# Kernel tuning notes

Hardware: AMD Instinct MI355X
Metric: run time of the kernel (lower is better)

## Reference

```python
import jax, jax.numpy as jnp
import numpy as np

B, L, D = 4, 1024, 1024
H, DK, DV = 16, 64, 64
HID = 4 * D
EPS = 1e-5


def layer_norm(x, w, b):
    m = x.mean(-1, keepdims=True)
    v = ((x - m) ** 2).mean(-1, keepdims=True)
    return (x - m) * jax.lax.rsqrt(v + EPS) * w + b


def sln(hl, w, ln_w, ln_b, gamma, beta):
    # Self-modulated LayerNorm: gamma * w * LN(hl) + beta * w
    return gamma * w * layer_norm(hl, ln_w, ln_b) + beta * w


def setup_inputs() -> dict:
    key = jax.random.key(0)
    ks = jax.random.split(key, 20)
    s = 0.02
    inp = {
        "q": jax.random.normal(ks[0], (B, L, D), jnp.float32),
        "k": jax.random.normal(ks[1], (B, L, D), jnp.float32),
        "v": jax.random.normal(ks[2], (B, L, D), jnp.float32),
        "z": jax.random.normal(ks[3], (B, L, D), jnp.float32),
        # projections stored [in, out] (torch Linear applies x @ W.T + b)
        "wq_w": jax.random.normal(ks[4], (D, H * DK), jnp.float32) * s,
        "wq_b": jnp.zeros((H * DK,), jnp.float32),
        "wk_w": jax.random.normal(ks[5], (D, H * DK), jnp.float32) * s,
        "wk_b": jnp.zeros((H * DK,), jnp.float32),
        "wv_w": jax.random.normal(ks[6], (D, H * DV), jnp.float32) * s,
        "wv_b": jnp.zeros((H * DV,), jnp.float32),
        "fc_w": jax.random.normal(ks[7], (H * DV, D), jnp.float32) * s,
        "fc_b": jnp.zeros((D,), jnp.float32),
        "mlp1_w": jax.random.normal(ks[8], (D, HID), jnp.float32) * s,
        "mlp1_b": jnp.zeros((HID,), jnp.float32),
        "mlp2_w": jax.random.normal(ks[9], (HID, D), jnp.float32) * s,
        "mlp2_b": jnp.zeros((D,), jnp.float32),
        "ln1_w": jnp.ones((D,), jnp.float32),
        "ln1_b": jnp.zeros((D,), jnp.float32),
        "g1": jax.random.normal(ks[10], (1, 1, 1), jnp.float32),
        "b1": jax.random.normal(ks[11], (1, 1, 1), jnp.float32),
        "ln2_w": jnp.ones((D,), jnp.float32),
        "ln2_b": jnp.zeros((D,), jnp.float32),
        "g2": jax.random.normal(ks[12], (1, 1, 1), jnp.float32),
        "b2": jax.random.normal(ks[13], (1, 1, 1), jnp.float32),
    }
    return inp


def reference(q, k, v, z,
              wq_w, wq_b, wk_w, wk_b, wv_w, wv_b, fc_w, fc_b,
              mlp1_w, mlp1_b, mlp2_w, mlp2_b,
              ln1_w, ln1_b, g1, b1, ln2_w, ln2_b, g2, b2):
    scale = 1.0 / np.sqrt(DK).astype(np.float32)
    q = sln(q, z, ln1_w, ln1_b, g1, b1)
    residual = q
    qh = (q @ wq_w + wq_b).reshape(B, L, H, DK)
    kh = (k @ wk_w + wk_b).reshape(B, L, H, DK)
    vh = (v @ wv_w + wv_b).reshape(B, L, H, DV)
    # scores per (head, batch) matching torch layout (n_head*sz_b, Lq, Lk)
    attn = jnp.einsum("bqhd,bkhd->hbqk", qh, kh) * scale
    attn = jax.nn.softmax(attn, axis=-1)
    out = jnp.einsum("hbqk,bkhd->bqhd", attn, vh).reshape(B, L, H * DV)
    out = out @ fc_w + fc_b
    out = out + residual
    h = sln(out, z, ln2_w, ln2_b, g2, b2)
    h = jax.nn.gelu(h @ mlp1_w + mlp1_b, approximate=False)
    out = (h @ mlp2_w + mlp2_b) + out
    return out, attn.reshape(H * B, L, L)
```

## Files before the change

kernel.cpp:

```cpp
#include <hip/hip_runtime.h>
#include <math.h>

namespace {

constexpr int kL  = 1024;
constexpr int kD  = 1024;
constexpr int kB  = 4;
constexpr int kH  = 16;
constexpr int kDK = 64;
constexpr int kHID = 4096;

typedef unsigned short ushort_t;
typedef short  s16x8 __attribute__((ext_vector_type(8)));
typedef float  f32x4 __attribute__((ext_vector_type(4)));
typedef unsigned short u16x4 __attribute__((ext_vector_type(4)));

__device__ __forceinline__ ushort_t f2bf(float f) {
    unsigned u = __float_as_uint(f);
    unsigned r = u + 0x7fffu + ((u >> 16) & 1u);
    return (ushort_t)(r >> 16);
}

__device__ __forceinline__ void gld16(const void* g, void* l) {
    __builtin_amdgcn_global_load_lds((__attribute__((address_space(1))) void*)(g),
                                     (__attribute__((address_space(3))) void*)(l),
                                     16, 0, 0);
}

__device__ __forceinline__ float wred_sum(float v) {
    #pragma unroll
    for (int o = 32; o > 0; o >>= 1) v += __shfl_xor(v, o, 64);
    return v;
}

__global__ __launch_bounds__(256) void sln_kernel(
    const float* __restrict__ x, const float* __restrict__ x2, float* __restrict__ xw,
    const float* __restrict__ z,
    const float* __restrict__ lnw, const float* __restrict__ lnb,
    const float* __restrict__ g, const float* __restrict__ bt,
    float* __restrict__ outf, ushort_t* __restrict__ outb)
{
    const int row = blockIdx.x;
    const int tid = threadIdx.x;
    const size_t base = (size_t)row * kD;
    float4 xv = ((const float4*)(x + base))[tid];
    if (x2) {
        float4 a = ((const float4*)(x2 + base))[tid];
        xv.x += a.x; xv.y += a.y; xv.z += a.z; xv.w += a.w;
    }
    if (xw) ((float4*)(xw + base))[tid] = xv;
    float s  = xv.x + xv.y + xv.z + xv.w;
    float sq = xv.x * xv.x + xv.y * xv.y + xv.z * xv.z + xv.w * xv.w;
    __shared__ float r1[4], r2[4];
    float ws = wred_sum(s), wq = wred_sum(sq);
    int lane = tid & 63, wid = tid >> 6;
    if (lane == 0) { r1[wid] = ws; r2[wid] = wq; }
    __syncthreads();
    float st = r1[0] + r1[1] + r1[2] + r1[3];
    float qt = r2[0] + r2[1] + r2[2] + r2[3];
    float mean = st * (1.0f / kD);
    float var  = qt * (1.0f / kD) - mean * mean;
    float rs = rsqrtf(var + 1e-5f);
    float gv = g[0], bv = bt[0];
    float4 zv = ((const float4*)(z + base))[tid];
    float4 wv = ((const float4*)lnw)[tid];
    float4 lb = ((const float4*)lnb)[tid];
    float4 o;
    o.x = zv.x * (gv * ((xv.x - mean) * rs * wv.x + lb.x) + bv);
    o.y = zv.y * (gv * ((xv.y - mean) * rs * wv.y + lb.y) + bv);
    o.z = zv.z * (gv * ((xv.z - mean) * rs * wv.z + lb.z) + bv);
    o.w = zv.w * (gv * ((xv.w - mean) * rs * wv.w + lb.w) + bv);
    if (outf) ((float4*)(outf + base))[tid] = o;
    u16x4 ob; ob[0] = f2bf(o.x); ob[1] = f2bf(o.y); ob[2] = f2bf(o.z); ob[3] = f2bf(o.w);
    ((u16x4*)(outb + base))[tid] = ob;
}

__global__ __launch_bounds__(256) void cvt2_bf16(
    const float* __restrict__ kx, const float* __restrict__ vx, ushort_t* __restrict__ kv)
{
    int b = blockIdx.x;
    bool isv = b >= 4096;
    const float* src = isv ? vx : kx;
    ushort_t* dst = kv + (isv ? (size_t)4194304 : 0);
    int i = (b & 4095) * 256 + threadIdx.x;
    f32x4 v = ((const f32x4*)src)[i];
    u16x4 o; o[0] = f2bf(v[0]); o[1] = f2bf(v[1]); o[2] = f2bf(v[2]); o[3] = f2bf(v[3]);
    ((u16x4*)dst)[i] = o;
}

__global__ __launch_bounds__(256) void addf4(
    float* __restrict__ dst, const float* __restrict__ src)
{
    int i = blockIdx.x * 256 + threadIdx.x;
    f32x4 d = ((const f32x4*)dst)[i];
    f32x4 s = ((const f32x4*)src)[i];
    d[0] += s[0]; d[1] += s[1]; d[2] += s[2]; d[3] += s[3];
    ((f32x4*)dst)[i] = d;
}

__global__ __launch_bounds__(256) void twcvt(
    const float* __restrict__ src, ushort_t* __restrict__ dst, int R, int C)
{
    __shared__ float t[32][33];
    int c0 = blockIdx.x * 32, r0 = blockIdx.y * 32;
    int tx = threadIdx.x & 31, ty = threadIdx.x >> 5;
    #pragma unroll
    for (int i = 0; i < 4; i++) {
        int r = ty + i * 8;
        t[r][tx] = src[(size_t)(r0 + r) * C + c0 + tx];
    }
    __syncthreads();
    #pragma unroll
    for (int i = 0; i < 4; i++) {
        int c = ty + i * 8;
        dst[(size_t)(c0 + c) * R + r0 + tx] = f2bf(t[tx][c]);
    }
}

__global__ __launch_bounds__(256) void twcvt4(
    const float* __restrict__ s0, const float* __restrict__ s1,
    const float* __restrict__ s2, const float* __restrict__ s3,
    ushort_t* __restrict__ dst)
{
    __shared__ float t[32][33];
    int zz = blockIdx.z;
    const float* src = zz == 0 ? s0 : zz == 1 ? s1 : zz == 2 ? s2 : s3;
    ushort_t* d = dst + (size_t)zz * 1048576;
    int c0 = blockIdx.x * 32, r0 = blockIdx.y * 32;
    int tx = threadIdx.x & 31, ty = threadIdx.x >> 5;
    #pragma unroll
    for (int i = 0; i < 4; i++) {
        int r = ty + i * 8;
        t[r][tx] = src[(size_t)(r0 + r) * 1024 + c0 + tx];
    }
    __syncthreads();
    #pragma unroll
    for (int i = 0; i < 4; i++) {
        int c = ty + i * 8;
        d[(size_t)(c0 + c) * 1024 + r0 + tx] = f2bf(t[tx][c]);
    }
}

__global__ __launch_bounds__(256) void vtrans(
    const ushort_t* __restrict__ vh, ushort_t* __restrict__ vhT)
{
    __shared__ ushort_t t[32][33];
    int p = blockIdx.z, b = p & 3, h = p >> 2;
    int j0 = blockIdx.x * 32, d0 = blockIdx.y * 32;
    int tx = threadIdx.x & 31, ty = threadIdx.x >> 5;
    const ushort_t* src = vh + (size_t)b * (kL * kD) + h * kDK;
    #pragma unroll
    for (int i = 0; i < 4; i++) {
        int j = ty + i * 8;
        t[j][tx] = src[(size_t)(j0 + j) * kD + d0 + tx];
    }
    __syncthreads();
    ushort_t* dst = vhT + (size_t)p * (kDK * kL);
    #pragma unroll
    for (int i = 0; i < 4; i++) {
        int d = ty + i * 8;
        dst[(size_t)(d0 + d) * kL + j0 + tx] = t[tx][d];
    }
}

__global__ __launch_bounds__(256) void mgemm(
    const ushort_t* __restrict__ A, int lda,
    const ushort_t* __restrict__ Bt, int ldb,
    void* __restrict__ Cv, int ldc, int K,
    const float* __restrict__ bias, const float* __restrict__ res,
    float scale, int flags, int mode,
    const float* __restrict__ bias1, const float* __restrict__ bias2,
    void* __restrict__ Cv2)
{
    __shared__ __align__(16) ushort_t As[128 * 32];
    __shared__ __align__(16) ushort_t Bs[128 * 32];
    if (mode == 2) {
        int z = blockIdx.z;
        A  += (size_t)z * (4096u * 1024u);
        Bt += (size_t)z * (1024u * 1024u);
        Cv = (void*)((ushort_t*)Cv + (size_t)z * (4096u * 1024u));
        if (z == 1) bias = bias1;
        else if (z == 2) bias = bias2;
    } else if (mode == 3) {
        int z = blockIdx.z;
        A  += (size_t)z * K;
        Bt += (size_t)z * K;
        if (z == 1) { Cv = Cv2; bias = nullptr; res = nullptr; flags = 0; }
    }
    float*    Cf = (float*)Cv;
    ushort_t* Cb = (ushort_t*)Cv;
    const int nx = gridDim.x, nwg = nx * gridDim.y;
    int f = blockIdx.y * nx + blockIdx.x;
    int rr = (f & 7) * (nwg >> 3) + (f >> 3);
    const int bx = rr % nx, by = rr / nx;
    const int tid = threadIdx.x;
    const int lane = tid & 63, w = tid >> 6;
    const int m0 = by * 128, n0 = bx * 128;
    const int r0 = tid >> 2;
    const int c0 = (tid & 3) ^ (r0 & 3);
    const ushort_t* Ag0 = A  + (size_t)(m0 + r0) * lda + c0 * 8;
    const ushort_t* Ag1 = Ag0 + (size_t)64 * lda;
    const ushort_t* Bg0 = Bt + (size_t)(n0 + r0) * ldb + c0 * 8;
    const ushort_t* Bg1 = Bg0 + (size_t)64 * ldb;
    char* AsW = (char*)As + w * 1024;
    char* BsW = (char*)Bs + w * 1024;
    const int wm = (w & 1) * 64, wn = (w >> 1) * 64;
    const int fn = lane & 15, q = lane >> 4;
    int aoff[4], boff[4];
    #pragma unroll
    for (int i = 0; i < 4; i++) {
        int ra = wm + i * 16 + fn;
        aoff[i] = (ra * 4 + (q ^ (ra & 3))) * 16;
        int rb = wn + i * 16 + fn;
        boff[i] = (rb * 4 + (q ^ (rb & 3))) * 16;
    }
    f32x4 acc[4][4] = {};
    for (int k0 = 0; k0 < K; k0 += 32) {
        gld16(Ag0 + k0, AsW);
        gld16(Ag1 + k0, AsW + 4096);
        gld16(Bg0 + k0, BsW);
        gld16(Bg1 + k0, BsW + 4096);
        __syncthreads();
        s16x8 af[4], bfr[4];
        #pragma unroll
        for (int i = 0; i < 4; i++) {
            af[i]  = *(const s16x8*)((const char*)As + aoff[i]);
            bfr[i] = *(const s16x8*)((const char*)Bs + boff[i]);
        }
        #pragma unroll
        for (int mi = 0; mi < 4; mi++)
            #pragma unroll
            for (int ni = 0; ni < 4; ni++)
                acc[mi][ni] = __builtin_amdgcn_mfma_f32_16x16x32_bf16(
                    af[mi], bfr[ni], acc[mi][ni], 0, 0, 0);
        __syncthreads();
    }
    #pragma unroll
    for (int mi = 0; mi < 4; mi++) {
        #pragma unroll
        for (int ni = 0; ni < 4; ni++) {
            #pragma unroll
            for (int r = 0; r < 4; r++) {
                int gm = m0 + wm + mi * 16 + q * 4 + r;
                int gn = n0 + wn + ni * 16 + fn;
                float v = acc[mi][ni][r] * scale;
                if (bias) v += bias[gn];
                if (flags & 1) v = 0.5f * v * (1.0f + erff(v * 0.70710678118654752f));
                if (res) v += res[(size_t)gm * ldc + gn];
                if (flags & 2) Cb[(size_t)gm * ldc + gn] = f2bf(v);
                else           Cf[(size_t)gm * ldc + gn] = v;
            }
        }
    }
}

__global__ __launch_bounds__(512) void fused_attn(
    const ushort_t* __restrict__ qh, const ushort_t* __restrict__ kh,
    const ushort_t* __restrict__ vhT, float* __restrict__ attn,
    ushort_t* __restrict__ ctx)
{
    __shared__ __align__(16) char PlBuf[8 * 4096];
    __shared__ float redm[8][32];
    __shared__ float reds[8][32];
    const int orig = blockIdx.y * 32 + blockIdx.x;
    const int nf = (orig & 7) * 256 + (orig >> 3);
    const int p = nf >> 5, b = p & 3, h = p >> 2;
    const int m0 = (nf & 31) * 32;
    const int tid = threadIdx.x;
    const int lane = tid & 63, w = tid >> 6;
    const int fn = lane & 15, q = lane >> 4;
    const ushort_t* Qb = qh + (size_t)b * (kL * kD) + h * 64;
    const ushort_t* Kb = kh + (size_t)b * (kL * kD) + h * 64;
    float* Pp = attn + (size_t)p * kL * kL;

    f32x4 acc[2][8] = {};
    #pragma unroll
    for (int kk = 0; kk < 2; kk++) {
        s16x8 aq[2], bq[8];
        #pragma unroll
        for (int mi = 0; mi < 2; mi++)
            aq[mi] = *(const s16x8*)(Qb + (size_t)(m0 + mi * 16 + fn) * kD + kk * 32 + q * 8);
        #pragma unroll
        for (int ni = 0; ni < 8; ni++)
            bq[ni] = *(const s16x8*)(Kb + (size_t)(w * 128 + ni * 16 + fn) * kD + kk * 32 + q * 8);
        #pragma unroll
        for (int mi = 0; mi < 2; mi++)
            #pragma unroll
            for (int ni = 0; ni < 8; ni++)
                acc[mi][ni] = __builtin_amdgcn_mfma_f32_16x16x32_bf16(
                    aq[mi], bq[ni], acc[mi][ni], 0, 0, 0);
    }

    float mloc[2][4];
    #pragma unroll
    for (int mi = 0; mi < 2; mi++) {
        #pragma unroll
        for (int r = 0; r < 4; r++) {
            float m = -3.0e38f;
            #pragma unroll
            for (int ni = 0; ni < 8; ni++) {
                acc[mi][ni][r] *= 0.125f;
                m = fmaxf(m, acc[mi][ni][r]);
            }
            mloc[mi][r] = m;
        }
    }
    #pragma unroll
    for (int o = 1; o < 16; o <<= 1) {
        #pragma unroll
        for (int mi = 0; mi < 2; mi++)
            #pragma unroll
            for (int r = 0; r < 4; r++)
                mloc[mi][r] = fmaxf(mloc[mi][r], __shfl_xor(mloc[mi][r], o, 64));
    }
    if (fn == 0) {
        #pragma unroll
        for (int mi = 0; mi < 2; mi++)
            #pragma unroll
            for (int r = 0; r < 4; r++)
                redm[w][mi * 16 + q * 4 + r] = mloc[mi][r];
    }
    __syncthreads();
    #pragma unroll
    for (int mi = 0; mi < 2; mi++) {
        #pragma unroll
        for (int r = 0; r < 4; r++) {
            int row = mi * 16 + q * 4 + r;
            float m = redm[0][row];
            #pragma unroll
            for (int w2 = 1; w2 < 8; w2++) m = fmaxf(m, redm[w2][row]);
            float s = 0.f;
            #pragma unroll
            for (int ni = 0; ni < 8; ni++) {
                float e = __expf(acc[mi][ni][r] - m);
                acc[mi][ni][r] = e;
                s += e;
            }
            mloc[mi][r] = s;
        }
    }
    #pragma unroll
    for (int o = 1; o < 16; o <<= 1) {
        #pragma unroll
        for (int mi = 0; mi < 2; mi++)
            #pragma unroll
            for (int r = 0; r < 4; r++)
                mloc[mi][r] += __shfl_xor(mloc[mi][r], o, 64);
    }
    if (fn == 0) {
        #pragma unroll
        for (int mi = 0; mi < 2; mi++)
            #pragma unroll
            for (int r = 0; r < 4; r++)
                reds[w][mi * 16 + q * 4 + r] = mloc[mi][r];
    }
    __syncthreads();
    float inv[2][4];
    #pragma unroll
    for (int mi = 0; mi < 2; mi++) {
        #pragma unroll
        for (int r = 0; r < 4; r++) {
            int row = mi * 16 + q * 4 + r;
            float s = reds[0][row];
            #pragma unroll
            for (int w2 = 1; w2 < 8; w2++) s += reds[w2][row];
            inv[mi][r] = 1.0f / s;
        }
    }
    #pragma unroll
    for (int mi = 0; mi < 2; mi++)
        #pragma unroll
        for (int ni = 0; ni < 8; ni++)
            #pragma unroll
            for (int r = 0; r < 4; r++)
                __builtin_nontemporal_store(
                    acc[mi][ni][r] * inv[mi][r],
                    &Pp[(size_t)(m0 + mi * 16 + q * 4 + r) * kL + w * 128 + ni * 16 + fn]);

    const ushort_t* Vb = vhT + (size_t)p * (kDK * kL);
    char* Plw = PlBuf + w * 4096;
    f32x4 acc2[2][4] = {};
    #pragma unroll
    for (int half = 0; half < 2; half++) {
        #pragma unroll
        for (int mi = 0; mi < 2; mi++)
            #pragma unroll
            for (int ni = 0; ni < 4; ni++)
                #pragma unroll
                for (int r = 0; r < 4; r++) {
                    int row = mi * 16 + q * 4 + r;
                    int cl  = ni * 16 + fn;
                    *(ushort_t*)(Plw + ((row * 128 + cl * 2) ^ ((row & 7) << 4)))
                        = f2bf(acc[mi][half * 4 + ni][r]);
                }
        #pragma unroll
        for (int kh2 = 0; kh2 < 2; kh2++) {
            int kk = half * 2 + kh2;
            s16x8 pa[2];
            #pragma unroll
            for (int mi = 0; mi < 2; mi++) {
                int row = mi * 16 + fn;
                pa[mi] = *(const s16x8*)(Plw +
                    ((row * 128 + (kh2 * 32 + q * 8) * 2) ^ ((row & 7) << 4)));
            }
            #pragma unroll
            for (int nj = 0; nj < 4; nj++) {
                s16x8 bv = *(const s16x8*)(Vb + (size_t)(nj * 16 + fn) * kL +
                                           w * 128 + kk * 32 + q * 8);
                #pragma unroll
                for (int mi = 0; mi < 2; mi++)
                    acc2[mi][nj] = __builtin_amdgcn_mfma_f32_16x16x32_bf16(
                        pa[mi], bv, acc2[mi][nj], 0, 0, 0);
            }
        }
    }
    #pragma unroll
    for (int mi = 0; mi < 2; mi++)
        #pragma unroll
        for (int nj = 0; nj < 4; nj++)
            #pragma unroll
            for (int r = 0; r < 4; r++)
                acc2[mi][nj][r] *= inv[mi][r];

    __syncthreads();
    float (*cred)[2048] = (float (*)[2048])PlBuf;
    if (w < 4) {
        #pragma unroll
        for (int mi = 0; mi < 2; mi++)
            #pragma unroll
            for (int nj = 0; nj < 4; nj++)
                #pragma unroll
                for (int r = 0; r < 4; r++)
                    cred[w][(mi * 16 + q * 4 + r) * 64 + nj * 16 + fn] = acc2[mi][nj][r];
    }
    __syncthreads();
    if (w >= 4) {
        #pragma unroll
        for (int mi = 0; mi < 2; mi++)
            #pragma unroll
            for (int nj = 0; nj < 4; nj++)
                #pragma unroll
                for (int r = 0; r < 4; r++)
                    cred[w - 4][(mi * 16 + q * 4 + r) * 64 + nj * 16 + fn] += acc2[mi][nj][r];
    }
    __syncthreads();
    {
        int idx0 = tid * 4;
        int row = idx0 >> 6, d0 = idx0 & 63;
        f32x4 s0 = *(const f32x4*)&cred[0][idx0];
        #pragma unroll
        for (int wb = 1; wb < 4; wb++) {
            f32x4 t = *(const f32x4*)&cred[wb][idx0];
            s0[0] += t[0]; s0[1] += t[1]; s0[2] += t[2]; s0[3] += t[3];
        }
        u16x4 o;
        o[0] = f2bf(s0[0]); o[1] = f2bf(s0[1]); o[2] = f2bf(s0[2]); o[3] = f2bf(s0[3]);
        *(u16x4*)(ctx + (size_t)b * (kL * kD) + (size_t)(m0 + row) * kD + h * 64 + d0) = o;
    }
}

}

extern "C" void kernel_launch(void* const* d_in, const int* in_sizes, int n_in,
                              void* d_out, int out_size, void* d_ws, size_t ws_size,
                              hipStream_t stream)
{
    (void)in_sizes; (void)n_in; (void)out_size; (void)ws_size;
    const float* q      = (const float*)d_in[0];
    const float* k      = (const float*)d_in[1];
    const float* v      = (const float*)d_in[2];
    const float* z      = (const float*)d_in[3];
    const float* wq_w   = (const float*)d_in[4];
    const float* wq_b   = (const float*)d_in[5];
    const float* wk_w   = (const float*)d_in[6];
    const float* wk_b   = (const float*)d_in[7];
    const float* wv_w   = (const float*)d_in[8];
    const float* wv_b   = (const float*)d_in[9];
    const float* fc_w   = (const float*)d_in[10];
    const float* fc_b   = (const float*)d_in[11];
    const float* mlp1_w = (const float*)d_in[12];
    const float* mlp1_b = (const float*)d_in[13];
    const float* mlp2_w = (const float*)d_in[14];
    const float* mlp2_b = (const float*)d_in[15];
    const float* ln1_w  = (const float*)d_in[16];
    const float* ln1_b  = (const float*)d_in[17];
    const float* g1     = (const float*)d_in[18];
    const float* b1     = (const float*)d_in[19];
    const float* ln2_w  = (const float*)d_in[20];
    const float* ln2_b  = (const float*)d_in[21];
    const float* g2     = (const float*)d_in[22];
    const float* b2     = (const float*)d_in[23];

    float* out0 = (float*)d_out;
    float* attn = (float*)d_out + (size_t)kB * kL * kD;

    char* arena = (char*)d_ws;
    const size_t MB = 1u << 20;
    float*    qp   = (float*)(arena);
    ushort_t* qb   = (ushort_t*)(arena + 16 * MB);
    ushort_t* kb   = (ushort_t*)(arena + 24 * MB);
    ushort_t* vb   = (ushort_t*)(arena + 32 * MB);
    ushort_t* qh   = (ushort_t*)(arena + 40 * MB);
    ushort_t* kh   = (ushort_t*)(arena + 48 * MB);
    ushort_t* vh   = (ushort_t*)(arena + 56 * MB);
    ushort_t* vhT  = (ushort_t*)(arena + 32 * MB);
    ushort_t* ctx  = (ushort_t*)(arena + 56 * MB);
    float*    fcP  = (float*)(arena + 16 * MB);
    ushort_t* h2   = (ushort_t*)(arena + 32 * MB);
    float*    out1 = (float*)(arena + 64 * MB);
    ushort_t* hid  = (ushort_t*)(arena);
    float*    m2P  = (float*)(arena + 40 * MB);
    ushort_t* wqT  = (ushort_t*)(arena + 80 * MB);
    ushort_t* fcT  = (ushort_t*)(arena + 86 * MB);
    ushort_t* m1T  = (ushort_t*)(arena + 88 * MB);
    ushort_t* m2T  = (ushort_t*)(arena + 96 * MB);

    dim3 blk(256);
    twcvt4<<<dim3(32, 32, 4), blk, 0, stream>>>(wq_w, wk_w, wv_w, fc_w, wqT);
    twcvt<<<dim3(128, 32), blk, 0, stream>>>(mlp1_w, m1T, kD, kHID);
    twcvt<<<dim3(32, 128), blk, 0, stream>>>(mlp2_w, m2T, kHID, kD);
    cvt2_bf16<<<dim3(8192), blk, 0, stream>>>(k, v, kb);
    sln_kernel<<<dim3(kB * kL), blk, 0, stream>>>(q, nullptr, nullptr, z,
                                                  ln1_w, ln1_b, g1, b1, qp, qb);
    mgemm<<<dim3(8, 32, 3), blk, 0, stream>>>(qb, kD, wqT, kD, qh, kD, kD,
                                              wq_b, nullptr, 1.0f, 2, 2, wk_b, wv_b, nullptr);
    vtrans<<<dim3(32, 2, 64), blk, 0, stream>>>(vh, vhT);
    fused_attn<<<dim3(kL / 32, 64), dim3(512), 0, stream>>>(qh, kh, vhT, attn, ctx);
    mgemm<<<dim3(8, 32, 2), blk, 0, stream>>>(ctx, kD, fcT, kD, out1, kD, kD / 2,
                                              fc_b, qp, 1.0f, 0, 3, nullptr, nullptr, fcP);
    sln_kernel<<<dim3(kB * kL), blk, 0, stream>>>(out1, fcP, out1, z,
                                                  ln2_w, ln2_b, g2, b2, nullptr, h2);
    mgemm<<<dim3(32, 32, 1), blk, 0, stream>>>(h2, kD, m1T, kD, hid, kHID, kD,
                                               mlp1_b, nullptr, 1.0f, 3, 0, nullptr, nullptr, nullptr);
    mgemm<<<dim3(8, 32, 2), blk, 0, stream>>>(hid, kHID, m2T, kHID, out0, kD, kHID / 2,
                                              mlp2_b, out1, 1.0f, 0, 3, nullptr, nullptr, m2P);
    addf4<<<dim3(4096), blk, 0, stream>>>(out0, m2P);
}
```

Baseline: 780.6 us.

## Add 256x256 triple-buffered GEMM kernel and merge preprocessing launches

```diff
diff --git a/kernel.cpp b/kernel.cpp
--- a/kernel.cpp
+++ b/kernel.cpp
@@ -31,6 +31,94 @@
     #pragma unroll
     for (int o = 32; o > 0; o >>= 1) v += __shfl_xor(v, o, 64);
     return v;
+}
+
+__global__ __launch_bounds__(256) void prep(
+    const float* __restrict__ wq_w, const float* __restrict__ wk_w,
+    const float* __restrict__ wv_w, const float* __restrict__ fc_w,
+    ushort_t* __restrict__ wT4,
+    const float* __restrict__ mlp1_w, ushort_t* __restrict__ m1T,
+    const float* __restrict__ mlp2_w, ushort_t* __restrict__ m2T,
+    const float* __restrict__ kx, const float* __restrict__ vx, ushort_t* __restrict__ kv,
+    const float* __restrict__ q, const float* __restrict__ z,
+    const float* __restrict__ ln1w, const float* __restrict__ ln1b,
+    const float* __restrict__ g1, const float* __restrict__ b1,
+    float* __restrict__ qp, ushort_t* __restrict__ qb)
+{
+    __shared__ float t[32][33];
+    __shared__ float r1[4], r2[4];
+    const int b = blockIdx.x;
+    const int tid = threadIdx.x;
+    if (b < 12288) {
+        const float* src; ushort_t* dst; int R, C, bx, by;
+        if (b < 4096) {
+            int zz = b >> 10, idx = b & 1023;
+            src = zz == 0 ? wq_w : zz == 1 ? wk_w : zz == 2 ? wv_w : fc_w;
+            dst = wT4 + (size_t)zz * 1048576;
+            R = 1024; C = 1024; bx = idx & 31; by = idx >> 5;
+        } else if (b < 8192) {
+            int idx = b - 4096;
+            src = mlp1_w; dst = m1T; R = 1024; C = 4096;
+            bx = idx & 127; by = idx >> 7;
+        } else {
+            int idx = b - 8192;
+            src = mlp2_w; dst = m2T; R = 4096; C = 1024;
+            bx = idx & 31; by = idx >> 5;
+        }
+        int c0 = bx * 32, rr0 = by * 32;
+        int tx = tid & 31, ty = tid >> 5;
+        #pragma unroll
+        for (int i = 0; i < 4; i++) {
+            int r = ty + i * 8;
+            t[r][tx] = src[(size_t)(rr0 + r) * C + c0 + tx];
+        }
+        __syncthreads();
+        #pragma unroll
+        for (int i = 0; i < 4; i++) {
+            int c = ty + i * 8;
+            dst[(size_t)(c0 + c) * R + rr0 + tx] = f2bf(t[tx][c]);
+        }
+        return;
+    }
+    if (b < 20480) {
+        int bb = b - 12288;
+        bool isv = bb >= 4096;
+        const float* src = isv ? vx : kx;
+        ushort_t* dst = kv + (isv ? (size_t)4194304 : 0);
+        int i = (bb & 4095) * 256 + tid;
+        f32x4 v = ((const f32x4*)src)[i];
+        u16x4 o; o[0] = f2bf(v[0]); o[1] = f2bf(v[1]); o[2] = f2bf(v[2]); o[3] = f2bf(v[3]);
+        ((u16x4*)dst)[i] = o;
+        return;
+    }
+    {
+        const int row = b - 20480;
+        const size_t base = (size_t)row * kD;
+        float4 xv = ((const float4*)(q + base))[tid];
+        float s  = xv.x + xv.y + xv.z + xv.w;
+        float sq = xv.x * xv.x + xv.y * xv.y + xv.z * xv.z + xv.w * xv.w;
+        float ws = wred_sum(s), wq = wred_sum(sq);
+        int lane = tid & 63, wid = tid >> 6;
+        if (lane == 0) { r1[wid] = ws; r2[wid] = wq; }
+        __syncthreads();
+        float st = r1[0] + r1[1] + r1[2] + r1[3];
+        float qt = r2[0] + r2[1] + r2[2] + r2[3];
+        float mean = st * (1.0f / kD);
+        float var  = qt * (1.0f / kD) - mean * mean;
+        float rs = rsqrtf(var + 1e-5f);
+        float gv = g1[0], bv = b1[0];
+        float4 zv = ((const float4*)(z + base))[tid];
+        float4 wv = ((const float4*)ln1w)[tid];
+        float4 lb = ((const float4*)ln1b)[tid];
+        float4 o;
+        o.x = zv.x * (gv * ((xv.x - mean) * rs * wv.x + lb.x) + bv);
+        o.y = zv.y * (gv * ((xv.y - mean) * rs * wv.y + lb.y) + bv);
+        o.z = zv.z * (gv * ((xv.z - mean) * rs * wv.z + lb.z) + bv);
+        o.w = zv.w * (gv * ((xv.w - mean) * rs * wv.w + lb.w) + bv);
+        ((float4*)(qp + base))[tid] = o;
+        u16x4 ob; ob[0] = f2bf(o.x); ob[1] = f2bf(o.y); ob[2] = f2bf(o.z); ob[3] = f2bf(o.w);
+        ((u16x4*)(qb + base))[tid] = ob;
+    }
 }
 
 __global__ __launch_bounds__(256) void sln_kernel(
@@ -75,70 +163,18 @@
     ((u16x4*)(outb + base))[tid] = ob;
 }
 
-__global__ __launch_bounds__(256) void cvt2_bf16(
-    const float* __restrict__ kx, const float* __restrict__ vx, ushort_t* __restrict__ kv)
-{
-    int b = blockIdx.x;
-    bool isv = b >= 4096;
-    const float* src = isv ? vx : kx;
-    ushort_t* dst = kv + (isv ? (size_t)4194304 : 0);
-    int i = (b & 4095) * 256 + threadIdx.x;
-    f32x4 v = ((const f32x4*)src)[i];
-    u16x4 o; o[0] = f2bf(v[0]); o[1] = f2bf(v[1]); o[2] = f2bf(v[2]); o[3] = f2bf(v[3]);
-    ((u16x4*)dst)[i] = o;
-}
-
-__global__ __launch_bounds__(256) void addf4(
-    float* __restrict__ dst, const float* __restrict__ src)
+__global__ __launch_bounds__(256) void combine4(
+    float* __restrict__ dst, const float* __restrict__ p1,
+    const float* __restrict__ p2, const float* __restrict__ p3)
 {
     int i = blockIdx.x * 256 + threadIdx.x;
     f32x4 d = ((const f32x4*)dst)[i];
-    f32x4 s = ((const f32x4*)src)[i];
-    d[0] += s[0]; d[1] += s[1]; d[2] += s[2]; d[3] += s[3];
+    f32x4 a = ((const f32x4*)p1)[i];
+    f32x4 b = ((const f32x4*)p2)[i];
+    f32x4 c = ((const f32x4*)p3)[i];
+    d[0] += a[0] + b[0] + c[0]; d[1] += a[1] + b[1] + c[1];
+    d[2] += a[2] + b[2] + c[2]; d[3] += a[3] + b[3] + c[3];
     ((f32x4*)dst)[i] = d;
-}
-
-__global__ __launch_bounds__(256) void twcvt(
-    const float* __restrict__ src, ushort_t* __restrict__ dst, int R, int C)
-{
-    __shared__ float t[32][33];
-    int c0 = blockIdx.x * 32, r0 = blockIdx.y * 32;
-    int tx = threadIdx.x & 31, ty = threadIdx.x >> 5;
-    #pragma unroll
-    for (int i = 0; i < 4; i++) {
-        int r = ty + i * 8;
-        t[r][tx] = src[(size_t)(r0 + r) * C + c0 + tx];
-    }
-    __syncthreads();
-    #pragma unroll
-    for (int i = 0; i < 4; i++) {
-        int c = ty + i * 8;
-        dst[(size_t)(c0 + c) * R + r0 + tx] = f2bf(t[tx][c]);
-    }
-}
-
-__global__ __launch_bounds__(256) void twcvt4(
-    const float* __restrict__ s0, const float* __restrict__ s1,
-    const float* __restrict__ s2, const float* __restrict__ s3,
-    ushort_t* __restrict__ dst)
-{
-    __shared__ float t[32][33];
-    int zz = blockIdx.z;
-    const float* src = zz == 0 ? s0 : zz == 1 ? s1 : zz == 2 ? s2 : s3;
-    ushort_t* d = dst + (size_t)zz * 1048576;
-    int c0 = blockIdx.x * 32, r0 = blockIdx.y * 32;
-    int tx = threadIdx.x & 31, ty = threadIdx.x >> 5;
-    #pragma unroll
-    for (int i = 0; i < 4; i++) {
-        int r = ty + i * 8;
-        t[r][tx] = src[(size_t)(r0 + r) * 1024 + c0 + tx];
-    }
-    __syncthreads();
-    #pragma unroll
-    for (int i = 0; i < 4; i++) {
-        int c = ty + i * 8;
-        d[(size_t)(c0 + c) * 1024 + r0 + tx] = f2bf(t[tx][c]);
-    }
 }
 
 __global__ __launch_bounds__(256) void vtrans(
@@ -174,14 +210,7 @@
 {
     __shared__ __align__(16) ushort_t As[128 * 32];
     __shared__ __align__(16) ushort_t Bs[128 * 32];
-    if (mode == 2) {
-        int z = blockIdx.z;
-        A  += (size_t)z * (4096u * 1024u);
-        Bt += (size_t)z * (1024u * 1024u);
-        Cv = (void*)((ushort_t*)Cv + (size_t)z * (4096u * 1024u));
-        if (z == 1) bias = bias1;
-        else if (z == 2) bias = bias2;
-    } else if (mode == 3) {
+    if (mode == 3) {
         int z = blockIdx.z;
         A  += (size_t)z * K;
         Bt += (size_t)z * K;
@@ -243,6 +272,130 @@
             for (int r = 0; r < 4; r++) {
                 int gm = m0 + wm + mi * 16 + q * 4 + r;
                 int gn = n0 + wn + ni * 16 + fn;
+                float v = acc[mi][ni][r] * scale;
+                if (bias) v += bias[gn];
+                if (flags & 1) v = 0.5f * v * (1.0f + erff(v * 0.70710678118654752f));
+                if (res) v += res[(size_t)gm * ldc + gn];
+                if (flags & 2) Cb[(size_t)gm * ldc + gn] = f2bf(v);
+                else           Cf[(size_t)gm * ldc + gn] = v;
+            }
+        }
+    }
+}
+
+__global__ __launch_bounds__(512, 2) void g3(
+    const ushort_t* __restrict__ A, int lda,
+    const ushort_t* __restrict__ Bt, int ldb,
+    void* __restrict__ Cv, int ldc, int K,
+    const float* __restrict__ bias, const float* __restrict__ res,
+    float scale, int flags, int mode,
+    const float* __restrict__ bias1, const float* __restrict__ bias2,
+    float* __restrict__ Cv2, float* __restrict__ Cv3)
+{
+    __shared__ __align__(16) ushort_t As[3 * 8192];
+    __shared__ __align__(16) ushort_t Bs[3 * 8192];
+    if (mode == 2) {
+        int zz = blockIdx.z;
+        A  += (size_t)zz * (4096u * 1024u);
+        Bt += (size_t)zz * (1024u * 1024u);
+        Cv = (void*)((ushort_t*)Cv + (size_t)zz * (4096u * 1024u));
+        if (zz == 1) bias = bias1;
+        else if (zz == 2) bias = bias2;
+    } else if (mode == 4) {
+        int zz = blockIdx.z;
+        A  += (size_t)zz * K;
+        Bt += (size_t)zz * K;
+        if (zz > 0) {
+            Cv = (void*)(zz == 3 ? Cv3 : (Cv2 + (size_t)(zz - 1) * (4096u * 1024u)));
+            bias = nullptr; res = nullptr; flags = 0;
+        }
+    }
+    float*    Cf = (float*)Cv;
+    ushort_t* Cb = (ushort_t*)Cv;
+    const int nx = gridDim.x, nwg = nx * gridDim.y;
+    int f = blockIdx.y * nx + blockIdx.x;
+    int rr = (f & 7) * (nwg >> 3) + (f >> 3);
+    const int bx = rr % nx, by = rr / nx;
+    const int tid = threadIdx.x;
+    const int lane = tid & 63, w = tid >> 6;
+    const int wr = w >> 2, wc = w & 3;
+    const int fn = lane & 15, q = lane >> 4;
+    const int m0 = by * 256, n0 = bx * 256;
+    const int r0 = tid >> 2;
+    const int c0 = (tid & 3) ^ (r0 & 3);
+    const ushort_t* Ag = A  + (size_t)(m0 + r0) * lda + c0 * 8;
+    const ushort_t* Bg = Bt + (size_t)(n0 + r0) * ldb + c0 * 8;
+    char* AsB = (char*)As;
+    char* BsB = (char*)Bs;
+    const int sdst = w * 1024;
+    int aoff[8], boff[4];
+    #pragma unroll
+    for (int i = 0; i < 8; i++) {
+        int ra = wr * 128 + i * 16 + fn;
+        aoff[i] = ra * 64 + ((q ^ (ra & 3)) << 4);
+    }
+    #pragma unroll
+    for (int i = 0; i < 4; i++) {
+        int rb = wc * 64 + i * 16 + fn;
+        boff[i] = rb * 64 + ((q ^ (rb & 3)) << 4);
+    }
+    const int NT = K >> 5;
+    f32x4 acc[8][4] = {};
+
+    #define G3_STAGE(T, s_, h_)                                                   \
+        do {                                                                      \
+            gld16(Ag + (size_t)((h_) * 128) * lda + (size_t)(T) * 32,             \
+                  AsB + (s_) * 16384 + (h_) * 8192 + sdst);                       \
+            gld16(Bg + (size_t)((h_) * 128) * ldb + (size_t)(T) * 32,             \
+                  BsB + (s_) * 16384 + (h_) * 8192 + sdst);                       \
+        } while (0)
+
+    G3_STAGE(0, 0, 0); G3_STAGE(0, 0, 1);
+    G3_STAGE(1, 1, 0); G3_STAGE(1, 1, 1);
+    asm volatile("s_waitcnt vmcnt(4)" ::: "memory");
+    __builtin_amdgcn_s_barrier();
+    __builtin_amdgcn_sched_barrier(0);
+
+    int sT = 0, s2 = 2;
+    for (int T = 0; T < NT; ++T) {
+        if (T + 2 < NT) { G3_STAGE(T + 2, s2, 0); G3_STAGE(T + 2, s2, 1); }
+        const char* Asl = (const char*)As + sT * 16384;
+        const char* Bsl = (const char*)Bs + sT * 16384;
+        s16x8 af[8], bf[4];
+        #pragma unroll
+        for (int i = 0; i < 8; i++) af[i] = *(const s16x8*)(Asl + aoff[i]);
+        #pragma unroll
+        for (int i = 0; i < 4; i++) bf[i] = *(const s16x8*)(Bsl + boff[i]);
+        asm volatile("s_waitcnt lgkmcnt(0)" ::: "memory");
+        __builtin_amdgcn_sched_barrier(0);
+        __builtin_amdgcn_s_setprio(1);
+        #pragma unroll
+        for (int mi = 0; mi < 8; mi++)
+            #pragma unroll
+            for (int ni = 0; ni < 4; ni++)
+                acc[mi][ni] = __builtin_amdgcn_mfma_f32_16x16x32_bf16(
+                    af[mi], bf[ni], acc[mi][ni], 0, 0, 0);
+        __builtin_amdgcn_s_setprio(0);
+        __builtin_amdgcn_sched_barrier(0);
+        if (T + 1 < NT) {
+            if (T + 2 < NT) asm volatile("s_waitcnt vmcnt(4)" ::: "memory");
+            else            asm volatile("s_waitcnt vmcnt(0)" ::: "memory");
+            __builtin_amdgcn_s_barrier();
+            __builtin_amdgcn_sched_barrier(0);
+        }
+        sT = (sT == 2) ? 0 : sT + 1;
+        s2 = (s2 == 2) ? 0 : s2 + 1;
+    }
+    #undef G3_STAGE
+
+    #pragma unroll
+    for (int mi = 0; mi < 8; mi++) {
+        #pragma unroll
+        for (int ni = 0; ni < 4; ni++) {
+            #pragma unroll
+            for (int r = 0; r < 4; r++) {
+                int gm = m0 + wr * 128 + mi * 16 + q * 4 + r;
+                int gn = n0 + wc * 64 + ni * 16 + fn;
                 float v = acc[mi][ni][r] * scale;
                 if (bias) v += bias[gn];
                 if (flags & 1) v = 0.5f * v * (1.0f + erff(v * 0.70710678118654752f));
@@ -509,30 +662,32 @@
     ushort_t* h2   = (ushort_t*)(arena + 32 * MB);
     float*    out1 = (float*)(arena + 64 * MB);
     ushort_t* hid  = (ushort_t*)(arena);
-    float*    m2P  = (float*)(arena + 40 * MB);
-    ushort_t* wqT  = (ushort_t*)(arena + 80 * MB);
+    float*    p1   = (float*)(arena + 32 * MB);
+    float*    p3   = (float*)(arena + 80 * MB);
+    ushort_t* wT4  = (ushort_t*)(arena + 80 * MB);
     ushort_t* fcT  = (ushort_t*)(arena + 86 * MB);
     ushort_t* m1T  = (ushort_t*)(arena + 88 * MB);
     ushort_t* m2T  = (ushort_t*)(arena + 96 * MB);
 
     dim3 blk(256);
-    twcvt4<<<dim3(32, 32, 4), blk, 0, stream>>>(wq_w, wk_w, wv_w, fc_w, wqT);
-    twcvt<<<dim3(128, 32), blk, 0, stream>>>(mlp1_w, m1T, kD, kHID);
-    twcvt<<<dim3(32, 128), blk, 0, stream>>>(mlp2_w, m2T, kHID, kD);
-    cvt2_bf16<<<dim3(8192), blk, 0, stream>>>(k, v, kb);
-    sln_kernel<<<dim3(kB * kL), blk, 0, stream>>>(q, nullptr, nullptr, z,
-                                                  ln1_w, ln1_b, g1, b1, qp, qb);
-    mgemm<<<dim3(8, 32, 3), blk, 0, stream>>>(qb, kD, wqT, kD, qh, kD, kD,
-                                              wq_b, nullptr, 1.0f, 2, 2, wk_b, wv_b, nullptr);
+    prep<<<dim3(24576), blk, 0, stream>>>(wq_w, wk_w, wv_w, fc_w, wT4,
+                                          mlp1_w, m1T, mlp2_w, m2T,
+                                          k, v, kb,
+                                          q, z, ln1_w, ln1_b, g1, b1, qp, qb);
+    g3<<<dim3(4, 16, 3), dim3(512), 0, stream>>>(qb, kD, wT4, kD, qh, kD, kD,
+                                                 wq_b, nullptr, 1.0f, 2, 2,
+                                                 wk_b, wv_b, nullptr, nullptr);
     vtrans<<<dim3(32, 2, 64), blk, 0, stream>>>(vh, vhT);
     fused_attn<<<dim3(kL / 32, 64), dim3(512), 0, stream>>>(qh, kh, vhT, attn, ctx);
     mgemm<<<dim3(8, 32, 2), blk, 0, stream>>>(ctx, kD, fcT, kD, out1, kD, kD / 2,
                                               fc_b, qp, 1.0f, 0, 3, nullptr, nullptr, fcP);
     sln_kernel<<<dim3(kB * kL), blk, 0, stream>>>(out1, fcP, out1, z,
                                                   ln2_w, ln2_b, g2, b2, nullptr, h2);
-    mgemm<<<dim3(32, 32, 1), blk, 0, stream>>>(h2, kD, m1T, kD, hid, kHID, kD,
-                                               mlp1_b, nullptr, 1.0f, 3, 0, nullptr, nullptr, nullptr);
-    mgemm<<<dim3(8, 32, 2), blk, 0, stream>>>(hid, kHID, m2T, kHID, out0, kD, kHID / 2,
-                                              mlp2_b, out1, 1.0f, 0, 3, nullptr, nullptr, m2P);
-    addf4<<<dim3(4096), blk, 0, stream>>>(out0, m2P);
-}
+    g3<<<dim3(16, 16, 1), dim3(512), 0, stream>>>(h2, kD, m1T, kD, hid, kHID, kD,
+                                                  mlp1_b, nullptr, 1.0f, 3, 0,
+                                                  nullptr, nullptr, nullptr, nullptr);
+    g3<<<dim3(4, 16, 4), dim3(512), 0, stream>>>(hid, kHID, m2T, kHID, out0, kD, kHID / 4,
+                                                 mlp2_b, out1, 1.0f, 0, 4,
+                                                 nullptr, nullptr, p1, p3);
+    combine4<<<dim3(4096), blk, 0, stream>>>(out0, p1, p1 + (size_t)4096 * 1024, p3);
+}
```

Result: slower. 822.3 us (+5.3%).

## Fuse prep kernels and compute V projection directly in transposed layout

Applied to the files above, without the earlier changes.

```diff
diff --git a/kernel.cpp b/kernel.cpp
--- a/kernel.cpp
+++ b/kernel.cpp
@@ -31,6 +31,94 @@
     #pragma unroll
     for (int o = 32; o > 0; o >>= 1) v += __shfl_xor(v, o, 64);
     return v;
+}
+
+__global__ __launch_bounds__(256) void prep(
+    const float* __restrict__ wq_w, const float* __restrict__ wk_w,
+    const float* __restrict__ wv_w, const float* __restrict__ fc_w,
+    ushort_t* __restrict__ wT4,
+    const float* __restrict__ mlp1_w, ushort_t* __restrict__ m1T,
+    const float* __restrict__ mlp2_w, ushort_t* __restrict__ m2T,
+    const float* __restrict__ kx, const float* __restrict__ vx, ushort_t* __restrict__ kv,
+    const float* __restrict__ q, const float* __restrict__ z,
+    const float* __restrict__ ln1w, const float* __restrict__ ln1b,
+    const float* __restrict__ g1, const float* __restrict__ b1,
+    float* __restrict__ qp, ushort_t* __restrict__ qb)
+{
+    __shared__ float t[32][33];
+    __shared__ float r1[4], r2[4];
+    const int b = blockIdx.x;
+    const int tid = threadIdx.x;
+    if (b < 12288) {
+        const float* src; ushort_t* dst; int R, C, bx, by;
+        if (b < 4096) {
+            int zz = b >> 10, idx = b & 1023;
+            src = zz == 0 ? wq_w : zz == 1 ? wk_w : zz == 2 ? wv_w : fc_w;
+            dst = wT4 + (size_t)zz * 1048576;
+            R = 1024; C = 1024; bx = idx & 31; by = idx >> 5;
+        } else if (b < 8192) {
+            int idx = b - 4096;
+            src = mlp1_w; dst = m1T; R = 1024; C = 4096;
+            bx = idx & 127; by = idx >> 7;
+        } else {
+            int idx = b - 8192;
+            src = mlp2_w; dst = m2T; R = 4096; C = 1024;
+            bx = idx & 31; by = idx >> 5;
+        }
+        int c0 = bx * 32, rr0 = by * 32;
+        int tx = tid & 31, ty = tid >> 5;
+        #pragma unroll
+        for (int i = 0; i < 4; i++) {
+            int r = ty + i * 8;
+            t[r][tx] = src[(size_t)(rr0 + r) * C + c0 + tx];
+        }
+        __syncthreads();
+        #pragma unroll
+        for (int i = 0; i < 4; i++) {
+            int c = ty + i * 8;
+            dst[(size_t)(c0 + c) * R + rr0 + tx] = f2bf(t[tx][c]);
+        }
+        return;
+    }
+    if (b < 20480) {
+        int bb = b - 12288;
+        bool isv = bb >= 4096;
+        const float* src = isv ? vx : kx;
+        ushort_t* dst = kv + (isv ? (size_t)4194304 : 0);
+        int i = (bb & 4095) * 256 + tid;
+        f32x4 v = ((const f32x4*)src)[i];
+        u16x4 o; o[0] = f2bf(v[0]); o[1] = f2bf(v[1]); o[2] = f2bf(v[2]); o[3] = f2bf(v[3]);
+        ((u16x4*)dst)[i] = o;
+        return;
+    }
+    {
+        const int row = b - 20480;
+        const size_t base = (size_t)row * kD;
+        float4 xv = ((const float4*)(q + base))[tid];
+        float s  = xv.x + xv.y + xv.z + xv.w;
+        float sq = xv.x * xv.x + xv.y * xv.y + xv.z * xv.z + xv.w * xv.w;
+        float ws = wred_sum(s), wq = wred_sum(sq);
+        int lane = tid & 63, wid = tid >> 6;
+        if (lane == 0) { r1[wid] = ws; r2[wid] = wq; }
+        __syncthreads();
+        float st = r1[0] + r1[1] + r1[2] + r1[3];
+        float qt = r2[0] + r2[1] + r2[2] + r2[3];
+        float mean = st * (1.0f / kD);
+        float var  = qt * (1.0f / kD) - mean * mean;
+        float rs = rsqrtf(var + 1e-5f);
+        float gv = g1[0], bv = b1[0];
+        float4 zv = ((const float4*)(z + base))[tid];
+        float4 wv = ((const float4*)ln1w)[tid];
+        float4 lb = ((const float4*)ln1b)[tid];
+        float4 o;
+        o.x = zv.x * (gv * ((xv.x - mean) * rs * wv.x + lb.x) + bv);
+        o.y = zv.y * (gv * ((xv.y - mean) * rs * wv.y + lb.y) + bv);
+        o.z = zv.z * (gv * ((xv.z - mean) * rs * wv.z + lb.z) + bv);
+        o.w = zv.w * (gv * ((xv.w - mean) * rs * wv.w + lb.w) + bv);
+        ((float4*)(qp + base))[tid] = o;
+        u16x4 ob; ob[0] = f2bf(o.x); ob[1] = f2bf(o.y); ob[2] = f2bf(o.z); ob[3] = f2bf(o.w);
+        ((u16x4*)(qb + base))[tid] = ob;
+    }
 }
 
 __global__ __launch_bounds__(256) void sln_kernel(
@@ -75,19 +163,6 @@
     ((u16x4*)(outb + base))[tid] = ob;
 }
 
-__global__ __launch_bounds__(256) void cvt2_bf16(
-    const float* __restrict__ kx, const float* __restrict__ vx, ushort_t* __restrict__ kv)
-{
-    int b = blockIdx.x;
-    bool isv = b >= 4096;
-    const float* src = isv ? vx : kx;
-    ushort_t* dst = kv + (isv ? (size_t)4194304 : 0);
-    int i = (b & 4095) * 256 + threadIdx.x;
-    f32x4 v = ((const f32x4*)src)[i];
-    u16x4 o; o[0] = f2bf(v[0]); o[1] = f2bf(v[1]); o[2] = f2bf(v[2]); o[3] = f2bf(v[3]);
-    ((u16x4*)dst)[i] = o;
-}
-
 __global__ __launch_bounds__(256) void addf4(
     float* __restrict__ dst, const float* __restrict__ src)
 {
@@ -98,94 +173,27 @@
     ((f32x4*)dst)[i] = d;
 }
 
-__global__ __launch_bounds__(256) void twcvt(
-    const float* __restrict__ src, ushort_t* __restrict__ dst, int R, int C)
-{
-    __shared__ float t[32][33];
-    int c0 = blockIdx.x * 32, r0 = blockIdx.y * 32;
-    int tx = threadIdx.x & 31, ty = threadIdx.x >> 5;
-    #pragma unroll
-    for (int i = 0; i < 4; i++) {
-        int r = ty + i * 8;
-        t[r][tx] = src[(size_t)(r0 + r) * C + c0 + tx];
-    }
-    __syncthreads();
-    #pragma unroll
-    for (int i = 0; i < 4; i++) {
-        int c = ty + i * 8;
-        dst[(size_t)(c0 + c) * R + r0 + tx] = f2bf(t[tx][c]);
-    }
-}
-
-__global__ __launch_bounds__(256) void twcvt4(
-    const float* __restrict__ s0, const float* __restrict__ s1,
-    const float* __restrict__ s2, const float* __restrict__ s3,
-    ushort_t* __restrict__ dst)
-{
-    __shared__ float t[32][33];
-    int zz = blockIdx.z;
-    const float* src = zz == 0 ? s0 : zz == 1 ? s1 : zz == 2 ? s2 : s3;
-    ushort_t* d = dst + (size_t)zz * 1048576;
-    int c0 = blockIdx.x * 32, r0 = blockIdx.y * 32;
-    int tx = threadIdx.x & 31, ty = threadIdx.x >> 5;
-    #pragma unroll
-    for (int i = 0; i < 4; i++) {
-        int r = ty + i * 8;
-        t[r][tx] = src[(size_t)(r0 + r) * 1024 + c0 + tx];
-    }
-    __syncthreads();
-    #pragma unroll
-    for (int i = 0; i < 4; i++) {
-        int c = ty + i * 8;
-        d[(size_t)(c0 + c) * 1024 + r0 + tx] = f2bf(t[tx][c]);
-    }
-}
-
-__global__ __launch_bounds__(256) void vtrans(
-    const ushort_t* __restrict__ vh, ushort_t* __restrict__ vhT)
-{
-    __shared__ ushort_t t[32][33];
-    int p = blockIdx.z, b = p & 3, h = p >> 2;
-    int j0 = blockIdx.x * 32, d0 = blockIdx.y * 32;
-    int tx = threadIdx.x & 31, ty = threadIdx.x >> 5;
-    const ushort_t* src = vh + (size_t)b * (kL * kD) + h * kDK;
-    #pragma unroll
-    for (int i = 0; i < 4; i++) {
-        int j = ty + i * 8;
-        t[j][tx] = src[(size_t)(j0 + j) * kD + d0 + tx];
-    }
-    __syncthreads();
-    ushort_t* dst = vhT + (size_t)p * (kDK * kL);
-    #pragma unroll
-    for (int i = 0; i < 4; i++) {
-        int d = ty + i * 8;
-        dst[(size_t)(d0 + d) * kL + j0 + tx] = t[tx][d];
-    }
-}
-
 __global__ __launch_bounds__(256) void mgemm(
     const ushort_t* __restrict__ A, int lda,
     const ushort_t* __restrict__ Bt, int ldb,
     void* __restrict__ Cv, int ldc, int K,
     const float* __restrict__ bias, const float* __restrict__ res,
     float scale, int flags, int mode,
-    const float* __restrict__ bias1, const float* __restrict__ bias2,
-    void* __restrict__ Cv2)
+    const float* __restrict__ bias1, void* __restrict__ Cv2)
 {
     __shared__ __align__(16) ushort_t As[128 * 32];
     __shared__ __align__(16) ushort_t Bs[128 * 32];
     if (mode == 2) {
-        int z = blockIdx.z;
-        A  += (size_t)z * (4096u * 1024u);
-        Bt += (size_t)z * (1024u * 1024u);
-        Cv = (void*)((ushort_t*)Cv + (size_t)z * (4096u * 1024u));
-        if (z == 1) bias = bias1;
-        else if (z == 2) bias = bias2;
+        int zz = blockIdx.z;
+        A  += (size_t)zz * (4096u * 1024u);
+        Bt += (size_t)zz * (1024u * 1024u);
+        Cv = (void*)((ushort_t*)Cv + (size_t)zz * (4096u * 1024u));
+        if (zz == 1) bias = bias1;
     } else if (mode == 3) {
-        int z = blockIdx.z;
-        A  += (size_t)z * K;
-        Bt += (size_t)z * K;
-        if (z == 1) { Cv = Cv2; bias = nullptr; res = nullptr; flags = 0; }
+        int zz = blockIdx.z;
+        A  += (size_t)zz * K;
+        Bt += (size_t)zz * K;
+        if (zz == 1) { Cv = Cv2; bias = nullptr; res = nullptr; flags = 0; }
     }
     float*    Cf = (float*)Cv;
     ushort_t* Cb = (ushort_t*)Cv;
@@ -244,7 +252,7 @@
                 int gm = m0 + wm + mi * 16 + q * 4 + r;
                 int gn = n0 + wn + ni * 16 + fn;
                 float v = acc[mi][ni][r] * scale;
-                if (bias) v += bias[gn];
+                if (bias) v += (flags & 4) ? bias[gm] : bias[gn];
                 if (flags & 1) v = 0.5f * v * (1.0f + erff(v * 0.70710678118654752f));
                 if (res) v += res[(size_t)gm * ldc + gn];
                 if (flags & 2) Cb[(size_t)gm * ldc + gn] = f2bf(v);
@@ -256,7 +264,7 @@
 
 __global__ __launch_bounds__(512) void fused_attn(
     const ushort_t* __restrict__ qh, const ushort_t* __restrict__ kh,
-    const ushort_t* __restrict__ vhT, float* __restrict__ attn,
+    const ushort_t* __restrict__ vT, float* __restrict__ attn,
     ushort_t* __restrict__ ctx)
 {
     __shared__ __align__(16) char PlBuf[8 * 4096];
@@ -377,7 +385,7 @@
                     acc[mi][ni][r] * inv[mi][r],
                     &Pp[(size_t)(m0 + mi * 16 + q * 4 + r) * kL + w * 128 + ni * 16 + fn]);
 
-    const ushort_t* Vb = vhT + (size_t)p * (kDK * kL);
+    const ushort_t* Vb = vT + (size_t)h * 64 * 4096 + (size_t)b * 1024;
     char* Plw = PlBuf + w * 4096;
     f32x4 acc2[2][4] = {};
     #pragma unroll
@@ -405,7 +413,7 @@
             }
             #pragma unroll
             for (int nj = 0; nj < 4; nj++) {
-                s16x8 bv = *(const s16x8*)(Vb + (size_t)(nj * 16 + fn) * kL +
+                s16x8 bv = *(const s16x8*)(Vb + (size_t)(nj * 16 + fn) * 4096 +
                                            w * 128 + kk * 32 + q * 8);
                 #pragma unroll
                 for (int mi = 0; mi < 2; mi++)
@@ -470,8 +478,8 @@
     const float* k      = (const float*)d_in[1];
     const float* v      = (const float*)d_in[2];
     const float* z      = (const float*)d_in[3];
+    const float* wq_b   = (const float*)d_in[5];
     const float* wq_w   = (const float*)d_in[4];
-    const float* wq_b   = (const float*)d_in[5];
     const float* wk_w   = (const float*)d_in[6];
     const float* wk_b   = (const float*)d_in[7];
     const float* wv_w   = (const float*)d_in[8];
@@ -502,37 +510,36 @@
     ushort_t* vb   = (ushort_t*)(arena + 32 * MB);
     ushort_t* qh   = (ushort_t*)(arena + 40 * MB);
     ushort_t* kh   = (ushort_t*)(arena + 48 * MB);
-    ushort_t* vh   = (ushort_t*)(arena + 56 * MB);
-    ushort_t* vhT  = (ushort_t*)(arena + 32 * MB);
-    ushort_t* ctx  = (ushort_t*)(arena + 56 * MB);
+    ushort_t* vT   = (ushort_t*)(arena + 56 * MB);
+    ushort_t* ctx  = (ushort_t*)(arena + 32 * MB);
     float*    fcP  = (float*)(arena + 16 * MB);
     ushort_t* h2   = (ushort_t*)(arena + 32 * MB);
     float*    out1 = (float*)(arena + 64 * MB);
     ushort_t* hid  = (ushort_t*)(arena);
     float*    m2P  = (float*)(arena + 40 * MB);
-    ushort_t* wqT  = (ushort_t*)(arena + 80 * MB);
+    ushort_t* wT4  = (ushort_t*)(arena + 80 * MB);
+    ushort_t* wvT  = (ushort_t*)(arena + 84 * MB);
     ushort_t* fcT  = (ushort_t*)(arena + 86 * MB);
     ushort_t* m1T  = (ushort_t*)(arena + 88 * MB);
     ushort_t* m2T  = (ushort_t*)(arena + 96 * MB);
 
     dim3 blk(256);
-    twcvt4<<<dim3(32, 32, 4), blk, 0, stream>>>(wq_w, wk_w, wv_w, fc_w, wqT);
-    twcvt<<<dim3(128, 32), blk, 0, stream>>>(mlp1_w, m1T, kD, kHID);
-    twcvt<<<dim3(32, 128), blk, 0, stream>>>(mlp2_w, m2T, kHID, kD);
-    cvt2_bf16<<<dim3(8192), blk, 0, stream>>>(k, v, kb);
-    sln_kernel<<<dim3(kB * kL), blk, 0, stream>>>(q, nullptr, nullptr, z,
-                                                  ln1_w, ln1_b, g1, b1, qp, qb);
-    mgemm<<<dim3(8, 32, 3), blk, 0, stream>>>(qb, kD, wqT, kD, qh, kD, kD,
-                                              wq_b, nullptr, 1.0f, 2, 2, wk_b, wv_b, nullptr);
-    vtrans<<<dim3(32, 2, 64), blk, 0, stream>>>(vh, vhT);
-    fused_attn<<<dim3(kL / 32, 64), dim3(512), 0, stream>>>(qh, kh, vhT, attn, ctx);
+    prep<<<dim3(24576), blk, 0, stream>>>(wq_w, wk_w, wv_w, fc_w, wT4,
+                                          mlp1_w, m1T, mlp2_w, m2T,
+                                          k, v, kb,
+                                          q, z, ln1_w, ln1_b, g1, b1, qp, qb);
+    mgemm<<<dim3(8, 32, 2), blk, 0, stream>>>(qb, kD, wT4, kD, qh, kD, kD,
+                                              wq_b, nullptr, 1.0f, 2, 2, wk_b, nullptr);
+    mgemm<<<dim3(32, 8, 1), blk, 0, stream>>>(wvT, kD, vb, kD, vT, 4096, kD,
+                                              wv_b, nullptr, 1.0f, 2 | 4, 0, nullptr, nullptr);
+    fused_attn<<<dim3(kL / 32, 64), dim3(512), 0, stream>>>(qh, kh, vT, attn, ctx);
     mgemm<<<dim3(8, 32, 2), blk, 0, stream>>>(ctx, kD, fcT, kD, out1, kD, kD / 2,
-                                              fc_b, qp, 1.0f, 0, 3, nullptr, nullptr, fcP);
+                                              fc_b, qp, 1.0f, 0, 3, nullptr, fcP);
     sln_kernel<<<dim3(kB * kL), blk, 0, stream>>>(out1, fcP, out1, z,
                                                   ln2_w, ln2_b, g2, b2, nullptr, h2);
     mgemm<<<dim3(32, 32, 1), blk, 0, stream>>>(h2, kD, m1T, kD, hid, kHID, kD,
-                                               mlp1_b, nullptr, 1.0f, 3, 0, nullptr, nullptr, nullptr);
+                                               mlp1_b, nullptr, 1.0f, 3, 0, nullptr, nullptr);
     mgemm<<<dim3(8, 32, 2), blk, 0, stream>>>(hid, kHID, m2T, kHID, out0, kD, kHID / 2,
-                                              mlp2_b, out1, 1.0f, 0, 3, nullptr, nullptr, m2P);
+                                              mlp2_b, out1, 1.0f, 0, 3, nullptr, m2P);
     addf4<<<dim3(4096), blk, 0, stream>>>(out0, m2P);
 }
```

Measured after the change: 798.3 us. 2.3% more time.
